# Performance work log

Hardware: AMD Instinct MI355X
Metric: run time of the kernel (lower is better)

Reference implementation:

```python
import jax, jax.numpy as jnp
import numpy as np

B, S, D = 4, 2048, 1024   # batch, seq_len, input feature dim
H, E = 16, 64             # head_num, att_embedding_size; H*E = model dim


def setup_inputs() -> dict:
    key = jax.random.key(0)
    ks = jax.random.split(key, 9)
    std = 1.0 / np.sqrt(D)
    M = H * E
    return {
        "x": jax.random.normal(ks[0], (B, S, D), dtype=jnp.float32),
        "Wq": jax.random.normal(ks[1], (D, M), dtype=jnp.float32) * std,
        "bq": jnp.zeros((M,), dtype=jnp.float32),
        "Wk": jax.random.normal(ks[2], (D, M), dtype=jnp.float32) * std,
        "bk": jnp.zeros((M,), dtype=jnp.float32),
        "Wv": jax.random.normal(ks[3], (D, M), dtype=jnp.float32) * std,
        "bv": jnp.zeros((M,), dtype=jnp.float32),
        "Wr": jax.random.normal(ks[4], (D, M), dtype=jnp.float32) * std,
        "br": jnp.zeros((M,), dtype=jnp.float32),
    }


def reference(x, Wq, bq, Wk, bk, Wv, bv, Wr, br):
    # QKV dense layers with ReLU activation (as in the original Keras code)
    qw = jax.nn.relu(x @ Wq + bq)                      # [B,S,H*E]
    kw = jax.nn.relu(x @ Wk + bk)
    vw = jax.nn.relu(x @ Wv + bv)
    # split heads: [B,S,H,E] -> [B,H,S,E]
    qw = qw.reshape(B, S, H, E).transpose(0, 2, 1, 3)
    kw = kw.reshape(B, S, H, E).transpose(0, 2, 1, 3)
    vw = vw.reshape(B, S, H, E).transpose(0, 2, 1, 3)
    # unscaled attention (original has no 1/sqrt(d) scaling)
    a = jnp.einsum("bhqe,bhke->bhqk", qw, kw)          # [B,H,S,S]
    a = jax.nn.softmax(a, axis=-1)
    o = jnp.einsum("bhqk,bhke->bhqe", a, vw)           # [B,H,S,E]
    o = o.transpose(0, 2, 1, 3).reshape(B, S, H * E)
    # residual dense (no activation)
    o = o + (x @ Wr + br)
    return o
```

## Files before the change

kernel.cpp:

```cpp
#include <hip/hip_runtime.h>


typedef __bf16 bf16x8 __attribute__((ext_vector_type(8)));
typedef float  f32x4  __attribute__((ext_vector_type(4)));
typedef short  short8 __attribute__((ext_vector_type(8)));
typedef short  short4v __attribute__((ext_vector_type(4)));
typedef float  float4v __attribute__((ext_vector_type(4)));
typedef int    int4v  __attribute__((ext_vector_type(4)));
typedef unsigned uint2v __attribute__((ext_vector_type(2)));

#define LOG2E 1.44269504088896f

__device__ __forceinline__ unsigned short f2bf(float f) {
  unsigned u = __builtin_bit_cast(unsigned, f);
  u += 0x7fffu + ((u >> 16) & 1u);
  return (unsigned short)(u >> 16);
}

__device__ __forceinline__ unsigned pack2(float lo, float hi) {
  __bf16 a = (__bf16)lo, b = (__bf16)hi;
  unsigned short ua = __builtin_bit_cast(unsigned short, a);
  unsigned short ub = __builtin_bit_cast(unsigned short, b);
  return (unsigned)ua | ((unsigned)ub << 16);
}

__global__ __launch_bounds__(256) void k_cvt_x(const float* __restrict__ x,
                                               short* __restrict__ Xb) {
  const size_t i = ((size_t)blockIdx.x * 256 + threadIdx.x) * 4;
  float4v f = *(const float4v*)(x + i);
  short4v o;
  o[0] = (short)f2bf(f[0]); o[1] = (short)f2bf(f[1]);
  o[2] = (short)f2bf(f[2]); o[3] = (short)f2bf(f[3]);
  *(short4v*)(Xb + i) = o;
}

__global__ __launch_bounds__(256) void k_cvt_w(const float* __restrict__ Wq,
                                               const float* __restrict__ Wk,
                                               const float* __restrict__ Wv,
                                               const float* __restrict__ Wr,
                                               short* __restrict__ Wc) {
  const int bid = blockIdx.x;
  const int w = bid >> 8;
  const int t = bid & 255;
  const int tr = t >> 4, tc = t & 15;
  const float* Ws = (w == 0) ? Wq : (w == 1) ? Wk : (w == 2) ? Wv : Wr;
  __shared__ float T[64][65];
  const int tx = threadIdx.x & 63, ty = threadIdx.x >> 6;
#pragma unroll
  for (int i = 0; i < 16; ++i)
    T[i * 4 + ty][tx] = Ws[(size_t)(tr * 64 + i * 4 + ty) * 1024 + tc * 64 + tx];
  __syncthreads();
#pragma unroll
  for (int i = 0; i < 16; ++i) {
    const int n = tc * 64 + i * 4 + ty;
    Wc[((size_t)w * 1024 + n) * 1024 + tr * 64 + tx] = (short)f2bf(T[tx][i * 4 + ty]);
  }
}

__global__ __launch_bounds__(256) void k_gemm(const short* __restrict__ Xb,
                                              const short* __restrict__ Wc,
                                              const float* __restrict__ bq,
                                              const float* __restrict__ bk2,
                                              const float* __restrict__ bv,
                                              const float* __restrict__ br,
                                              short* __restrict__ Qb,
                                              short* __restrict__ Kb,
                                              short* __restrict__ Vt,
                                              float* __restrict__ Out) {
  __shared__ short As[128 * 32];
  __shared__ short Bs[128 * 32];
  const int tid = threadIdx.x, wid = tid >> 6, lane = tid & 63;
  const int lr = lane & 15, hi = lane >> 4;
  const int bm = blockIdx.x & 63, bn = blockIdx.x >> 6;
  const int m0 = bm * 128, n0 = bn * 128;
  const int wr = wid >> 1, wc = wid & 1;

  f32x4 acc[4][4] = {};

  const int c0 = wid * 2;
  const int srow = lane >> 2;
  const int scol = (lane & 3) * 8;

  for (int k0 = 0; k0 < 1024; k0 += 32) {
    __syncthreads();
    const short* a0 = Xb + (size_t)(m0 + c0 * 16 + srow) * 1024 + k0 + scol;
    const short* a1 = Xb + (size_t)(m0 + (c0 + 1) * 16 + srow) * 1024 + k0 + scol;
    const short* b0 = Wc + (size_t)(n0 + c0 * 16 + srow) * 1024 + k0 + scol;
    const short* b1 = Wc + (size_t)(n0 + (c0 + 1) * 16 + srow) * 1024 + k0 + scol;
    __builtin_amdgcn_global_load_lds((const __attribute__((address_space(1))) void*)a0,
                                     (__attribute__((address_space(3))) void*)&As[c0 * 512], 16, 0, 0);
    __builtin_amdgcn_global_load_lds((const __attribute__((address_space(1))) void*)a1,
                                     (__attribute__((address_space(3))) void*)&As[(c0 + 1) * 512], 16, 0, 0);
    __builtin_amdgcn_global_load_lds((const __attribute__((address_space(1))) void*)b0,
                                     (__attribute__((address_space(3))) void*)&Bs[c0 * 512], 16, 0, 0);
    __builtin_amdgcn_global_load_lds((const __attribute__((address_space(1))) void*)b1,
                                     (__attribute__((address_space(3))) void*)&Bs[(c0 + 1) * 512], 16, 0, 0);
    __syncthreads();

    bf16x8 af[4], bfr[4];
#pragma unroll
    for (int i = 0; i < 4; ++i)
      af[i] = *(const bf16x8*)&As[(wr * 64 + i * 16 + lr) * 32 + hi * 8];
#pragma unroll
    for (int j = 0; j < 4; ++j)
      bfr[j] = *(const bf16x8*)&Bs[(wc * 64 + j * 16 + lr) * 32 + hi * 8];
#pragma unroll
    for (int i = 0; i < 4; ++i)
#pragma unroll
      for (int j = 0; j < 4; ++j)
        acc[i][j] = __builtin_amdgcn_mfma_f32_16x16x32_bf16(af[i], bfr[j], acc[i][j], 0, 0, 0);
  }

#pragma unroll
  for (int i = 0; i < 4; ++i) {
    const int mbase = m0 + wr * 64 + i * 16 + hi * 4;
    const int bb = mbase >> 11, sbase = mbase & 2047;
#pragma unroll
    for (int j = 0; j < 4; ++j) {
      const int n = n0 + wc * 64 + j * 16 + lr;
      const float* bp = (n < 2048) ? (n < 1024 ? bq : bk2) : (n < 3072 ? bv : br);
      const float bias = bp[n & 1023];
      float v[4];
#pragma unroll
      for (int r = 0; r < 4; ++r) v[r] = acc[i][j][r] + bias;

      if (n < 2048) {
        const int nn = n & 1023, h = nn >> 6, e = nn & 63;
        short* dst = (n < 1024) ? Qb : Kb;
#pragma unroll
        for (int r = 0; r < 4; ++r)
          dst[(((size_t)bb * 16 + h) * 2048 + sbase + r) * 64 + e] = (short)f2bf(fmaxf(v[r], 0.f));
      } else if (n < 3072) {
        const int nn = n & 1023, h = nn >> 6, e = nn & 63;
        const int kq = sbase & 31;
        const int Sp = (sbase & ~31) + ((kq >> 2) & 3) * 8 + (kq >> 4) * 4;
        uint2v pv;
        pv[0] = pack2(fmaxf(v[0], 0.f), fmaxf(v[1], 0.f));
        pv[1] = pack2(fmaxf(v[2], 0.f), fmaxf(v[3], 0.f));
        *(uint2v*)&Vt[(((size_t)bb * 16 + h) * 64 + e) * 2048 + Sp] = pv;
      } else {
#pragma unroll
        for (int r = 0; r < 4; ++r)
          Out[(size_t)(mbase + r) * 1024 + (n - 3072)] = v[r];
      }
    }
  }
}

__global__ __launch_bounds__(256, 2) void k_attn(const short* __restrict__ Qb,
                                                 const short* __restrict__ Kb,
                                                 const short* __restrict__ Vt,
                                                 float* __restrict__ Out) {
  __shared__ __align__(16) short smem[16384];
  char* const sb = (char*)smem;
  const int tid = threadIdx.x, wid = tid >> 6, lane = tid & 63;
  const int lr = lane & 15, hi = lane >> 4;
  const int bid = ((blockIdx.x & 7) << 6) | (blockIdx.x >> 3);
  const int bh = bid >> 3;
  const int q0 = (bid & 7) * 256;
  const size_t hb = (size_t)bh * (2048 * 64);

  bf16x8 aq[4][2];
#pragma unroll
  for (int g = 0; g < 4; ++g) {
    const short* qp = Qb + hb + (size_t)(q0 + wid * 64 + g * 16 + lr) * 64 + hi * 8;
    aq[g][0] = *(const bf16x8*)qp;
    aq[g][1] = *(const bf16x8*)(qp + 32);
  }

  f32x4 o[4][4] = {};
  float l_run[4] = {0.f, 0.f, 0.f, 0.f};

  const int swz = ((lane & 7) ^ (lane >> 3)) * 8;
  const int rlo = lane >> 3;
  const int wr0 = wid * 16;
  const short* kp0 = Kb + hb + (size_t)(wr0 + rlo) * 64 + swz;
  const short* kp1 = kp0 + 8 * 64;
  const short* vp0 = Vt + hb + (size_t)(wr0 + rlo) * 2048 + swz;
  const short* vp1 = vp0 + 8 * 2048;

  const int vb0 = (lr * 64 + ((hi ^ (lr & 7)) << 3)) * 2;
  const int vb1 = vb0 ^ 64;

#define GLL(SRC, LDSOFF)                                                                   \
  __builtin_amdgcn_global_load_lds((const __attribute__((address_space(1))) void*)(SRC),   \
      (__attribute__((address_space(3))) void*)(sb + (LDSOFF)), 16, 0, 0)

  GLL(kp0, wr0 * 128);
  GLL(kp1, wr0 * 128 + 1024);
  GLL(vp0, 16384 + wr0 * 128);
  GLL(vp1, 16384 + wr0 * 128 + 1024);
  kp0 += 4096; kp1 += 4096; vp0 += 64; vp1 += 64;

  for (int kt = 0; kt < 32; ++kt) {
    const int buf = kt & 1;
    if (kt < 31) {
      const int d = (buf ^ 1) * 8192 + wr0 * 128;
      GLL(kp0, d);
      GLL(kp1, d + 1024);
      GLL(vp0, 16384 + d);
      GLL(vp1, 16384 + d + 1024);
      kp0 += 4096; kp1 += 4096; vp0 += 64; vp1 += 64;
      asm volatile("s_waitcnt vmcnt(4)" ::: "memory");
    } else {
      asm volatile("s_waitcnt vmcnt(0)" ::: "memory");
    }
    __builtin_amdgcn_sched_barrier(0);
    __builtin_amdgcn_s_barrier();
    __builtin_amdgcn_sched_barrier(0);

    f32x4 s[4][4];
    __builtin_amdgcn_s_setprio(1);
#pragma unroll
    for (int kc = 0; kc < 4; ++kc) {
      const bf16x8 kf0 = *(const bf16x8*)(sb + (vb0 + buf * 8192 + kc * 2048));
      const bf16x8 kf1 = *(const bf16x8*)(sb + (vb1 + buf * 8192 + kc * 2048));
#pragma unroll
      for (int g = 0; g < 4; ++g) {
        f32x4 t = __builtin_amdgcn_mfma_f32_16x16x32_bf16(kf0, aq[g][0], (f32x4){0.f, 0.f, 0.f, 0.f}, 0, 0, 0);
        s[g][kc] = __builtin_amdgcn_mfma_f32_16x16x32_bf16(kf1, aq[g][1], t, 0, 0, 0);
      }
    }
    __builtin_amdgcn_s_setprio(0);

    int4v pw[4][2];
#pragma unroll
    for (int g = 0; g < 4; ++g) {
      float sum = 0.f;
#pragma unroll
      for (int kc = 0; kc < 4; ++kc) {
        const float p0 = __builtin_amdgcn_exp2f(s[g][kc][0] * LOG2E);
        const float p1 = __builtin_amdgcn_exp2f(s[g][kc][1] * LOG2E);
        const float p2 = __builtin_amdgcn_exp2f(s[g][kc][2] * LOG2E);
        const float p3 = __builtin_amdgcn_exp2f(s[g][kc][3] * LOG2E);
        sum += (p0 + p1) + (p2 + p3);
        pw[g][kc >> 1][(kc & 1) * 2] = (int)pack2(p0, p1);
        pw[g][kc >> 1][(kc & 1) * 2 + 1] = (int)pack2(p2, p3);
      }
      l_run[g] += sum;
    }

    __builtin_amdgcn_s_setprio(1);
#pragma unroll
    for (int kk = 0; kk < 2; ++kk) {
      const int cb = (kk ? vb1 : vb0) + 16384 + buf * 8192;
#pragma unroll
      for (int et = 0; et < 4; ++et) {
        const bf16x8 vf = *(const bf16x8*)(sb + (cb + et * 2048));
#pragma unroll
        for (int g = 0; g < 4; ++g)
          o[g][et] = __builtin_amdgcn_mfma_f32_16x16x32_bf16(
              vf, __builtin_bit_cast(bf16x8, pw[g][kk]), o[g][et], 0, 0, 0);
      }
    }
    __builtin_amdgcn_s_setprio(0);

    asm volatile("s_waitcnt lgkmcnt(0)" ::: "memory");
    __builtin_amdgcn_sched_barrier(0);
    __builtin_amdgcn_s_barrier();
    __builtin_amdgcn_sched_barrier(0);
  }

  float* Ep = (float*)smem + wid * 1088;
  const int b = bh >> 4, h = bh & 15;
  const int qr = lane >> 2, cc = lane & 3;
#pragma unroll
  for (int g = 0; g < 4; ++g) {
    float lt = l_run[g];
    lt += __shfl_xor(lt, 16);
    lt += __shfl_xor(lt, 32);
    const float inv = 1.0f / lt;
#pragma unroll
    for (int et = 0; et < 4; ++et) {
      f32x4 v = o[g][et] * inv;
      *(float4v*)&Ep[lr * 68 + et * 16 + hi * 4] = v;
    }
    asm volatile("s_waitcnt lgkmcnt(0)" ::: "memory");
    const size_t gb = ((size_t)b * 2048 + q0 + wid * 64 + g * 16 + qr) * 1024 + h * 64 + cc * 4;
#pragma unroll
    for (int i = 0; i < 4; ++i) {
      float4v v = *(const float4v*)&Ep[qr * 68 + cc * 4 + i * 16];
      float4v u = *(const float4v*)&Out[gb + i * 16];
      u += v;
      *(float4v*)&Out[gb + i * 16] = u;
    }
    asm volatile("s_waitcnt lgkmcnt(0)" ::: "memory");
  }
#undef GLL
}

extern "C" void kernel_launch(void* const* d_in, const int* in_sizes, int n_in,
                              void* d_out, int out_size, void* d_ws, size_t ws_size,
                              hipStream_t stream) {
  const float* x  = (const float*)d_in[0];
  const float* Wq = (const float*)d_in[1];
  const float* bq = (const float*)d_in[2];
  const float* Wk = (const float*)d_in[3];
  const float* bk = (const float*)d_in[4];
  const float* Wv = (const float*)d_in[5];
  const float* bv = (const float*)d_in[6];
  const float* Wr = (const float*)d_in[7];
  const float* br = (const float*)d_in[8];
  float* Out = (float*)d_out;

  char* ws = (char*)d_ws;
  short* Xb = (short*)(ws);
  short* Wc = (short*)(ws + (size_t)16 * 1024 * 1024);
  short* Qb = (short*)(ws + (size_t)24 * 1024 * 1024);
  short* Kb = (short*)(ws + (size_t)40 * 1024 * 1024);
  short* Vt = (short*)(ws + (size_t)56 * 1024 * 1024);

  k_cvt_x<<<8192, 256, 0, stream>>>(x, Xb);
  k_cvt_w<<<1024, 256, 0, stream>>>(Wq, Wk, Wv, Wr, Wc);
  k_gemm<<<2048, 256, 0, stream>>>(Xb, Wc, bq, bk, bv, br, Qb, Kb, Vt, Out);
  k_attn<<<512, 256, 0, stream>>>(Qb, Kb, Vt, Out);
}
```

Baseline: 189.2 us.

## Double-buffer LDS tiles in projection GEMM to overlap global loads with MFMA

```diff
diff --git a/kernel.cpp b/kernel.cpp
--- a/kernel.cpp
+++ b/kernel.cpp
@@ -67,8 +67,8 @@
                                               short* __restrict__ Kb,
                                               short* __restrict__ Vt,
                                               float* __restrict__ Out) {
-  __shared__ short As[128 * 32];
-  __shared__ short Bs[128 * 32];
+  __shared__ __align__(16) short smem[16384];
+  char* const sb = (char*)smem;
   const int tid = threadIdx.x, wid = tid >> 6, lane = tid & 63;
   const int lr = lane & 15, hi = lane >> 4;
   const int bm = blockIdx.x & 63, bn = blockIdx.x >> 6;
@@ -81,40 +81,65 @@
   const int srow = lane >> 2;
   const int scol = (lane & 3) * 8;
 
-  for (int k0 = 0; k0 < 1024; k0 += 32) {
-    __syncthreads();
-    const short* a0 = Xb + (size_t)(m0 + c0 * 16 + srow) * 1024 + k0 + scol;
-    const short* a1 = Xb + (size_t)(m0 + (c0 + 1) * 16 + srow) * 1024 + k0 + scol;
-    const short* b0 = Wc + (size_t)(n0 + c0 * 16 + srow) * 1024 + k0 + scol;
-    const short* b1 = Wc + (size_t)(n0 + (c0 + 1) * 16 + srow) * 1024 + k0 + scol;
-    __builtin_amdgcn_global_load_lds((const __attribute__((address_space(1))) void*)a0,
-                                     (__attribute__((address_space(3))) void*)&As[c0 * 512], 16, 0, 0);
-    __builtin_amdgcn_global_load_lds((const __attribute__((address_space(1))) void*)a1,
-                                     (__attribute__((address_space(3))) void*)&As[(c0 + 1) * 512], 16, 0, 0);
-    __builtin_amdgcn_global_load_lds((const __attribute__((address_space(1))) void*)b0,
-                                     (__attribute__((address_space(3))) void*)&Bs[c0 * 512], 16, 0, 0);
-    __builtin_amdgcn_global_load_lds((const __attribute__((address_space(1))) void*)b1,
-                                     (__attribute__((address_space(3))) void*)&Bs[(c0 + 1) * 512], 16, 0, 0);
-    __syncthreads();
+  const short* pa0 = Xb + (size_t)(m0 + c0 * 16 + srow) * 1024 + scol;
+  const short* pa1 = pa0 + 16 * 1024;
+  const short* pb0 = Wc + (size_t)(n0 + c0 * 16 + srow) * 1024 + scol;
+  const short* pb1 = pb0 + 16 * 1024;
+
+  const int ab = (wr * 64 + lr) * 64 + hi * 16;
+  const int bb = 16384 + (wc * 64 + lr) * 64 + hi * 16;
+
+#define GLL(SRC, LDSOFF)                                                                   \
+  __builtin_amdgcn_global_load_lds((const __attribute__((address_space(1))) void*)(SRC),   \
+      (__attribute__((address_space(3))) void*)(sb + (LDSOFF)), 16, 0, 0)
+
+  GLL(pa0, c0 * 1024);
+  GLL(pa1, c0 * 1024 + 1024);
+  GLL(pb0, 16384 + c0 * 1024);
+  GLL(pb1, 16384 + c0 * 1024 + 1024);
+  pa0 += 32; pa1 += 32; pb0 += 32; pb1 += 32;
+
+  for (int kt = 0; kt < 32; ++kt) {
+    const int buf = kt & 1;
+    if (kt < 31) {
+      const int d = (buf ^ 1) * 8192 + c0 * 1024;
+      GLL(pa0, d);
+      GLL(pa1, d + 1024);
+      GLL(pb0, 16384 + d);
+      GLL(pb1, 16384 + d + 1024);
+      pa0 += 32; pa1 += 32; pb0 += 32; pb1 += 32;
+      asm volatile("s_waitcnt vmcnt(4)" ::: "memory");
+    } else {
+      asm volatile("s_waitcnt vmcnt(0)" ::: "memory");
+    }
+    __builtin_amdgcn_sched_barrier(0);
+    __builtin_amdgcn_s_barrier();
+    __builtin_amdgcn_sched_barrier(0);
 
     bf16x8 af[4], bfr[4];
 #pragma unroll
     for (int i = 0; i < 4; ++i)
-      af[i] = *(const bf16x8*)&As[(wr * 64 + i * 16 + lr) * 32 + hi * 8];
+      af[i] = *(const bf16x8*)(sb + (buf * 8192 + ab + i * 1024));
 #pragma unroll
     for (int j = 0; j < 4; ++j)
-      bfr[j] = *(const bf16x8*)&Bs[(wc * 64 + j * 16 + lr) * 32 + hi * 8];
+      bfr[j] = *(const bf16x8*)(sb + (buf * 8192 + bb + j * 1024));
 #pragma unroll
     for (int i = 0; i < 4; ++i)
 #pragma unroll
       for (int j = 0; j < 4; ++j)
         acc[i][j] = __builtin_amdgcn_mfma_f32_16x16x32_bf16(af[i], bfr[j], acc[i][j], 0, 0, 0);
-  }
+
+    asm volatile("s_waitcnt lgkmcnt(0)" ::: "memory");
+    __builtin_amdgcn_sched_barrier(0);
+    __builtin_amdgcn_s_barrier();
+    __builtin_amdgcn_sched_barrier(0);
+  }
+#undef GLL
 
 #pragma unroll
   for (int i = 0; i < 4; ++i) {
     const int mbase = m0 + wr * 64 + i * 16 + hi * 4;
-    const int bb = mbase >> 11, sbase = mbase & 2047;
+    const int bb2 = mbase >> 11, sbase = mbase & 2047;
 #pragma unroll
     for (int j = 0; j < 4; ++j) {
       const int n = n0 + wc * 64 + j * 16 + lr;
@@ -129,7 +154,7 @@
         short* dst = (n < 1024) ? Qb : Kb;
 #pragma unroll
         for (int r = 0; r < 4; ++r)
-          dst[(((size_t)bb * 16 + h) * 2048 + sbase + r) * 64 + e] = (short)f2bf(fmaxf(v[r], 0.f));
+          dst[(((size_t)bb2 * 16 + h) * 2048 + sbase + r) * 64 + e] = (short)f2bf(fmaxf(v[r], 0.f));
       } else if (n < 3072) {
         const int nn = n & 1023, h = nn >> 6, e = nn & 63;
         const int kq = sbase & 31;
@@ -137,7 +162,7 @@
         uint2v pv;
         pv[0] = pack2(fmaxf(v[0], 0.f), fmaxf(v[1], 0.f));
         pv[1] = pack2(fmaxf(v[2], 0.f), fmaxf(v[3], 0.f));
-        *(uint2v*)&Vt[(((size_t)bb * 16 + h) * 64 + e) * 2048 + Sp] = pv;
+        *(uint2v*)&Vt[(((size_t)bb2 * 16 + h) * 64 + e) * 2048 + Sp] = pv;
       } else {
 #pragma unroll
         for (int r = 0; r < 4; ++r)
```

After: 194.9 us. 3.0% more time.

## Rewrite projection GEMM with 256x256 tiles and 4-stage async LDS pipeline

Applied to the files above, without the earlier changes.

```diff
diff --git a/kernel.cpp b/kernel.cpp
--- a/kernel.cpp
+++ b/kernel.cpp
@@ -57,79 +57,114 @@
   }
 }
 
-__global__ __launch_bounds__(256) void k_gemm(const short* __restrict__ Xb,
-                                              const short* __restrict__ Wc,
-                                              const float* __restrict__ bq,
-                                              const float* __restrict__ bk2,
-                                              const float* __restrict__ bv,
-                                              const float* __restrict__ br,
-                                              short* __restrict__ Qb,
-                                              short* __restrict__ Kb,
-                                              short* __restrict__ Vt,
-                                              float* __restrict__ Out) {
-  __shared__ short As[128 * 32];
-  __shared__ short Bs[128 * 32];
+__global__ __launch_bounds__(512, 2) void k_gemm(const short* __restrict__ Xb,
+                                                 const short* __restrict__ Wc,
+                                                 const float* __restrict__ bq,
+                                                 const float* __restrict__ bk2,
+                                                 const float* __restrict__ bv,
+                                                 const float* __restrict__ br,
+                                                 short* __restrict__ Qb,
+                                                 short* __restrict__ Kb,
+                                                 short* __restrict__ Vt,
+                                                 float* __restrict__ Out) {
+  __shared__ __align__(16) short smem[65536];
+  char* const sb = (char*)smem;
   const int tid = threadIdx.x, wid = tid >> 6, lane = tid & 63;
   const int lr = lane & 15, hi = lane >> 4;
-  const int bm = blockIdx.x & 63, bn = blockIdx.x >> 6;
-  const int m0 = bm * 128, n0 = bn * 128;
-  const int wr = wid >> 1, wc = wid & 1;
-
-  f32x4 acc[4][4] = {};
-
-  const int c0 = wid * 2;
-  const int srow = lane >> 2;
-  const int scol = (lane & 3) * 8;
-
-  for (int k0 = 0; k0 < 1024; k0 += 32) {
-    __syncthreads();
-    const short* a0 = Xb + (size_t)(m0 + c0 * 16 + srow) * 1024 + k0 + scol;
-    const short* a1 = Xb + (size_t)(m0 + (c0 + 1) * 16 + srow) * 1024 + k0 + scol;
-    const short* b0 = Wc + (size_t)(n0 + c0 * 16 + srow) * 1024 + k0 + scol;
-    const short* b1 = Wc + (size_t)(n0 + (c0 + 1) * 16 + srow) * 1024 + k0 + scol;
-    __builtin_amdgcn_global_load_lds((const __attribute__((address_space(1))) void*)a0,
-                                     (__attribute__((address_space(3))) void*)&As[c0 * 512], 16, 0, 0);
-    __builtin_amdgcn_global_load_lds((const __attribute__((address_space(1))) void*)a1,
-                                     (__attribute__((address_space(3))) void*)&As[(c0 + 1) * 512], 16, 0, 0);
-    __builtin_amdgcn_global_load_lds((const __attribute__((address_space(1))) void*)b0,
-                                     (__attribute__((address_space(3))) void*)&Bs[c0 * 512], 16, 0, 0);
-    __builtin_amdgcn_global_load_lds((const __attribute__((address_space(1))) void*)b1,
-                                     (__attribute__((address_space(3))) void*)&Bs[(c0 + 1) * 512], 16, 0, 0);
-    __syncthreads();
-
-    bf16x8 af[4], bfr[4];
-#pragma unroll
-    for (int i = 0; i < 4; ++i)
-      af[i] = *(const bf16x8*)&As[(wr * 64 + i * 16 + lr) * 32 + hi * 8];
-#pragma unroll
-    for (int j = 0; j < 4; ++j)
-      bfr[j] = *(const bf16x8*)&Bs[(wc * 64 + j * 16 + lr) * 32 + hi * 8];
-#pragma unroll
-    for (int i = 0; i < 4; ++i)
-#pragma unroll
-      for (int j = 0; j < 4; ++j)
-        acc[i][j] = __builtin_amdgcn_mfma_f32_16x16x32_bf16(af[i], bfr[j], acc[i][j], 0, 0, 0);
-  }
-
-#pragma unroll
-  for (int i = 0; i < 4; ++i) {
-    const int mbase = m0 + wr * 64 + i * 16 + hi * 4;
-    const int bb = mbase >> 11, sbase = mbase & 2047;
-#pragma unroll
-    for (int j = 0; j < 4; ++j) {
-      const int n = n0 + wc * 64 + j * 16 + lr;
+  const int bm = blockIdx.x & 31, bn = blockIdx.x >> 5;
+  const int m0 = bm * 256, n0 = bn * 256;
+  const int wm = wid >> 2, wn = wid & 3;
+
+  f32x4 acc[8][4] = {};
+
+  const int sl_ = (tid & 7) ^ ((tid >> 3) & 7);
+  const int rA0 = ((tid >> 3) << 1) + (sl_ >> 2);
+  const short* sa0 = Xb + (size_t)(m0 + rA0) * 1024 + (sl_ & 3) * 8;
+  const short* sa1 = Xb + (size_t)(m0 + 128 + rA0) * 1024 + (sl_ & 3) * 8;
+  const short* sg0 = Wc + (size_t)(n0 + rA0) * 1024 + (sl_ & 3) * 8;
+  const short* sg1 = Wc + (size_t)(n0 + 128 + rA0) * 1024 + (sl_ & 3) * 8;
+
+  const int xr = (((lane & 1) * 4 + hi) ^ ((lr >> 1) & 7)) * 16;
+  const int amb = wm * 8192 + (lr >> 1) * 128 + xr;
+  const int bnb = 65536 + wn * 4096 + (lr >> 1) * 128 + xr;
+
+#define GLL(SRC, LDSOFF)                                                                   \
+  __builtin_amdgcn_global_load_lds((const __attribute__((address_space(1))) void*)(SRC),   \
+      (__attribute__((address_space(3))) void*)(sb + (LDSOFF)), 16, 0, 0)
+
+#define STAGE(SLOT)                                                                        \
+  do {                                                                                     \
+    GLL(sa0, (SLOT) * 16384 + wid * 1024);                                                 \
+    GLL(sa1, (SLOT) * 16384 + 8192 + wid * 1024);                                          \
+    GLL(sg0, 65536 + (SLOT) * 16384 + wid * 1024);                                         \
+    GLL(sg1, 65536 + (SLOT) * 16384 + 8192 + wid * 1024);                                  \
+    sa0 += 32; sa1 += 32; sg0 += 32; sg1 += 32;                                            \
+  } while (0)
+
+#define PHASE(J, VM, STG)                                                                  \
+  do {                                                                                     \
+    asm volatile("s_waitcnt vmcnt(" #VM ")" ::: "memory");                                 \
+    __builtin_amdgcn_sched_barrier(0);                                                     \
+    __builtin_amdgcn_s_barrier();                                                          \
+    __builtin_amdgcn_sched_barrier(0);                                                     \
+    if (STG) STAGE(((J) + 3) & 3);                                                         \
+    bf16x8 am[8], bnr[4];                                                                  \
+    _Pragma("unroll")                                                                      \
+    for (int mf = 0; mf < 8; ++mf)                                                         \
+      am[mf] = *(const bf16x8*)(sb + (((J) & 3) * 16384 + amb + mf * 1024));               \
+    _Pragma("unroll")                                                                      \
+    for (int nf = 0; nf < 4; ++nf)                                                         \
+      bnr[nf] = *(const bf16x8*)(sb + (((J) & 3) * 16384 + bnb + nf * 1024));              \
+    asm volatile("s_waitcnt lgkmcnt(0)" ::: "memory");                                     \
+    __builtin_amdgcn_sched_barrier(0);                                                     \
+    __builtin_amdgcn_s_setprio(1);                                                         \
+    _Pragma("unroll")                                                                      \
+    for (int mf = 0; mf < 8; ++mf)                                                         \
+      _Pragma("unroll")                                                                    \
+      for (int nf = 0; nf < 4; ++nf)                                                       \
+        acc[mf][nf] = __builtin_amdgcn_mfma_f32_16x16x32_bf16(am[mf], bnr[nf],             \
+                                                              acc[mf][nf], 0, 0, 0);      \
+    __builtin_amdgcn_s_setprio(0);                                                         \
+    __builtin_amdgcn_sched_barrier(0);                                                     \
+  } while (0)
+
+  STAGE(0);
+  STAGE(1);
+  STAGE(2);
+
+  for (int it = 0; it < 7; ++it) {
+    PHASE(0, 8, 1);
+    PHASE(1, 8, 1);
+    PHASE(2, 8, 1);
+    PHASE(3, 8, 1);
+  }
+  PHASE(0, 8, 1);
+  PHASE(1, 8, 0);
+  PHASE(2, 4, 0);
+  PHASE(3, 0, 0);
+#undef PHASE
+#undef STAGE
+#undef GLL
+
+#pragma unroll
+  for (int mf = 0; mf < 8; ++mf) {
+    const int mbase = m0 + wm * 128 + mf * 16 + hi * 4;
+    const int bb2 = mbase >> 11, sbase = mbase & 2047;
+#pragma unroll
+    for (int nf = 0; nf < 4; ++nf) {
+      const int n = n0 + wn * 64 + nf * 16 + lr;
       const float* bp = (n < 2048) ? (n < 1024 ? bq : bk2) : (n < 3072 ? bv : br);
       const float bias = bp[n & 1023];
       float v[4];
 #pragma unroll
-      for (int r = 0; r < 4; ++r) v[r] = acc[i][j][r] + bias;
+      for (int r = 0; r < 4; ++r) v[r] = acc[mf][nf][r] + bias;
 
       if (n < 2048) {
         const int nn = n & 1023, h = nn >> 6, e = nn & 63;
         short* dst = (n < 1024) ? Qb : Kb;
 #pragma unroll
         for (int r = 0; r < 4; ++r)
-          dst[(((size_t)bb * 16 + h) * 2048 + sbase + r) * 64 + e] = (short)f2bf(fmaxf(v[r], 0.f));
+          dst[(((size_t)bb2 * 16 + h) * 2048 + sbase + r) * 64 + e] = (short)f2bf(fmaxf(v[r], 0.f));
       } else if (n < 3072) {
         const int nn = n & 1023, h = nn >> 6, e = nn & 63;
         const int kq = sbase & 31;
@@ -137,7 +172,7 @@
         uint2v pv;
         pv[0] = pack2(fmaxf(v[0], 0.f), fmaxf(v[1], 0.f));
         pv[1] = pack2(fmaxf(v[2], 0.f), fmaxf(v[3], 0.f));
-        *(uint2v*)&Vt[(((size_t)bb * 16 + h) * 64 + e) * 2048 + Sp] = pv;
+        *(uint2v*)&Vt[(((size_t)bb2 * 16 + h) * 64 + e) * 2048 + Sp] = pv;
       } else {
 #pragma unroll
         for (int r = 0; r < 4; ++r)
@@ -312,6 +347,6 @@
 
   k_cvt_x<<<8192, 256, 0, stream>>>(x, Xb);
   k_cvt_w<<<1024, 256, 0, stream>>>(Wq, Wk, Wv, Wr, Wc);
-  k_gemm<<<2048, 256, 0, stream>>>(Xb, Wc, bq, bk, bv, br, Qb, Kb, Vt, Out);
+  k_gemm<<<512, 512, 0, stream>>>(Xb, Wc, bq, bk, bv, br, Qb, Kb, Vt, Out);
   k_attn<<<512, 256, 0, stream>>>(Qb, Kb, Vt, Out);
 }
```

Measured after the change: 172.8 us. -8.7%, faster.
